# Kernel tuning notes

Hardware: AMD Instinct MI355X
Metric: run time of the kernel (lower is better)

The kernel has to match this reference:

```python
import jax, jax.numpy as jnp
import numpy as np


def _conv1(x, w, b):
    # 1x1x1 Conv3d on [B, C, T, H, W]: pure channel mixing.
    return jnp.einsum('bcthw,oc->bothw', x, w) + b[None, :, None, None, None]


def setup_inputs() -> dict:
    key = jax.random.key(0)
    B, T, C, H, W = 4, 7, 64, 64, 64
    C2 = C // 2  # nf // scale
    ks = jax.random.split(key, 16)
    inp = {"x": jax.random.normal(ks[0], (B, T, C, H, W), jnp.float32)}
    i = 1
    for p in ("hw", "c", "t"):
        for name in ("theta", "phi", "g"):
            inp[f"{p}_{name}_w"] = jax.random.normal(ks[i], (C2, C), jnp.float32) * 0.05
            inp[f"{p}_{name}_b"] = jnp.zeros((C2,), jnp.float32)
            i += 1
        inp[f"{p}_z_w"] = jax.random.normal(ks[i], (C, C2), jnp.float32) * 0.05
        inp[f"{p}_z_b"] = jnp.zeros((C,), jnp.float32)
        i += 1
    return inp


def reference(x, hw_theta_w, hw_theta_b, hw_phi_w, hw_phi_b, hw_g_w, hw_g_b,
              hw_z_w, hw_z_b, c_theta_w, c_theta_b, c_phi_w, c_phi_b,
              c_g_w, c_g_b, c_z_w, c_z_b, t_theta_w, t_theta_b,
              t_phi_w, t_phi_b, t_g_w, t_g_b, t_z_w, t_z_b):
    B, T, C, H, W = x.shape
    HW = H * W
    xc = jnp.transpose(x, (0, 2, 1, 3, 4))  # [B, C, T, H, W]

    # ---- spatial (HW) non-local: tokens are H*W positions, feature dim C2*T ----
    th = _conv1(xc, hw_theta_w, hw_theta_b).reshape(B, -1, HW)  # [B, C2*T, HW]
    ph = _conv1(xc, hw_phi_w, hw_phi_b).reshape(B, -1, HW)
    g = _conv1(xc, hw_g_w, hw_g_b).reshape(B, -1, HW)
    f = jax.nn.softmax(jnp.einsum('bkp,bkq->bpq', th, ph), axis=-1)  # [B, HW, HW]
    y = jnp.einsum('bpq,bkq->bkp', f, g).reshape(B, -1, T, H, W)
    hw_z = _conv1(y, hw_z_w, hw_z_b)

    # ---- channel (C) non-local: tokens are C2 channels, feature dim T*H*W ----
    th = _conv1(xc, c_theta_w, c_theta_b).reshape(B, -1, T * HW)  # [B, C2, THW]
    ph = _conv1(xc, c_phi_w, c_phi_b).reshape(B, -1, T * HW)
    g = _conv1(xc, c_g_w, c_g_b).reshape(B, -1, T * HW)
    f = jax.nn.softmax(jnp.einsum('bin,bjn->bij', th, ph), axis=-1)  # [B, C2, C2]
    y = jnp.einsum('bij,bjn->bin', f, g).reshape(B, -1, T, H, W)
    c_z = _conv1(y, c_z_w, c_z_b)

    # ---- temporal (T) non-local: tokens are T frames, feature dim C2*H*W ----
    th = jnp.transpose(_conv1(xc, t_theta_w, t_theta_b), (0, 2, 1, 3, 4)).reshape(B, T, -1)
    ph = jnp.transpose(_conv1(xc, t_phi_w, t_phi_b), (0, 2, 1, 3, 4)).reshape(B, T, -1)
    g = jnp.transpose(_conv1(xc, t_g_w, t_g_b), (0, 2, 1, 3, 4)).reshape(B, T, -1)
    f = jax.nn.softmax(jnp.einsum('btd,bsd->bts', th, ph), axis=-1)  # [B, T, T]
    y = jnp.einsum('bts,bsd->btd', f, g).reshape(B, T, -1, H, W)
    t_z = _conv1(jnp.transpose(y, (0, 2, 1, 3, 4)), t_z_w, t_z_b)

    z = hw_z + c_z + t_z + xc  # [B, C, T, H, W]
    return jnp.transpose(z, (0, 2, 1, 3, 4))  # [B, T, C, H, W]
```

## Files before the change

### kernel.cpp

```cpp
#include <hip/hip_runtime.h>
#include <hip/hip_bf16.h>

typedef unsigned short u16;
typedef __attribute__((ext_vector_type(8))) short s16x8;
typedef __attribute__((ext_vector_type(4))) float f32x4;

#define B_    4
#define T_    7
#define C_    64
#define C2_   32
#define HW_   4096
#define KF_   224
#define NTOT_ 28672

__device__ __forceinline__ float bf2f(u16 v){ return __uint_as_float(((unsigned)v)<<16); }
__device__ __forceinline__ u16 f2bf(float f){
  unsigned u = __float_as_uint(f);
  u = u + 0x7fffu + ((u>>16)&1u);
  return (u16)(u>>16);
}

static const size_t OFF_TH_HW=0;
static const size_t OFF_PH_HW=7340032;
static const size_t OFF_G_HW =14680064;
static const size_t OFF_Y_HW =22020096;
static const size_t OFF_TH_T =29360128;
static const size_t OFF_PH_T =44040192;
static const size_t OFF_GRAM =58720256;
static const size_t OFF_SROW =58785792;
static const size_t OFF_LT   =58786816;
static const size_t OFF_MC   =58787840;
static const size_t OFF_VC   =58853376;
static const size_t OFF_MT   =58854400;
static const size_t OFF_VT   =58870784;

__global__ __launch_bounds__(256) void k1_proj(
    const float* __restrict__ x,
    const float* w0,const float* bb0,const float* w1,const float* bb1,
    const float* w2,const float* bb2,const float* w3,const float* bb3,
    const float* w4,const float* bb4,
    u16* o0,u16* o1,u16* o2,float* o3,float* o4)
{
  __shared__ float wsm[5][C2_][C_];
  __shared__ float bsm[5][C2_];
  const float* wp[5]={w0,w1,w2,w3,w4};
  const float* bp[5]={bb0,bb1,bb2,bb3,bb4};
  int tid=threadIdx.x;
  for(int e=tid;e<5*C2_*C_;e+=256){ int pr=e>>11; int rc=e&2047; wsm[pr][rc>>6][rc&63]=wp[pr][rc]; }
  if(tid<5*C2_) bsm[tid>>5][tid&31]=bp[tid>>5][tid&31];
  __syncthreads();
  int bi=blockIdx.x;
  int b=bi/112, r=bi%112, t=r>>4;
  int p=((r&15)<<8)+tid;
  const float* xp = x + (((long)(b*T_+t))*C_)*HW_ + p;
  float xc[C_];
  #pragma unroll
  for(int c=0;c<C_;c++) xc[c]=xp[(long)c*HW_];
  long okm  = ((long)b*KF_ + t)*HW_ + p;
  long otok = ((long)(b*HW_) + p)*KF_ + t;

  for(int pr=0;pr<5;pr++){
    for(int c2=0;c2<C2_;c2++){
      float acc=bsm[pr][c2];
      const float4* wr=(const float4*)wsm[pr][c2];
      #pragma unroll
      for(int q=0;q<16;q++){ float4 w4=wr[q];
        acc+=w4.x*xc[q*4]+w4.y*xc[q*4+1]+w4.z*xc[q*4+2]+w4.w*xc[q*4+3]; }
      if(pr==0)      o0[otok + c2*T_]=f2bf(acc);
      else if(pr==1) o1[otok + c2*T_]=f2bf(acc);
      else if(pr==2) o2[okm + (long)(c2*T_)*HW_]=f2bf(acc);
      else if(pr==3) o3[okm + (long)(c2*T_)*HW_]=acc;
      else           o4[okm + (long)(c2*T_)*HW_]=acc;
    }
  }
}

__global__ __launch_bounds__(256,2) void k2_attn(
    const u16* __restrict__ th_tok,
    const u16* __restrict__ ph_tok,
    const u16* __restrict__ g_km,
    u16* __restrict__ y_g)
{
  __shared__ __align__(16) u16 ph_s[64][228];
  __shared__ __align__(16) u16 g_s[224][68];
  __shared__ float den_s[64];
  int tid=threadIdx.x;
  int id=blockIdx.x;
  int b=(id&7)>>1;
  int n=((id>>3)<<1)|(id&1);
  int p0=n<<6;
  int lane=tid&63, wv=tid>>6;
  int qw=wv<<4;
  int m=lane&15, gq=lane>>4;

  s16x8 thB[7];
  {
    const u16* thp = th_tok + ((long)(b*HW_ + p0 + qw + m))*KF_ + 4*gq;
    #pragma unroll
    for(int st=0; st<7; st++){
      union { s16x8 v; uint2 d[2]; } u;
      u.d[0]=*(const uint2*)(thp + st*32);
      u.d[1]=*(const uint2*)(thp + st*32 + 16);
      thB[st]=u.v;
    }
  }

  f32x4 Yacc[14];
  #pragma unroll
  for(int ft=0;ft<14;ft++) Yacc[ft]=(f32x4){0.f,0.f,0.f,0.f};
  float denp=0.f;

  const u16* phb = ph_tok + ((long)(b*HW_))*KF_;
  const u16* gb  = g_km  + ((long)(b*KF_))*HW_;

  int prow=tid>>2, pc0=(tid&3)*56;
  int gro=tid>>3,  gc0=(tid&7)*8;
  uint4 rph[7], rg[7];

  #pragma unroll
  for(int q=0;q<7;q++) rph[q]=*(const uint4*)(phb + (long)prow*KF_ + pc0 + q*8);
  #pragma unroll
  for(int it=0;it<7;it++) rg[it]=*(const uint4*)(gb + (long)(it*32+gro)*HW_ + gc0);

  for(int tile=0; tile<64; tile++){
    __syncthreads();
    { u16* dst=&ph_s[prow][pc0];
      #pragma unroll
      for(int q=0;q<7;q++){
        *(uint2*)(dst+q*8)  =make_uint2(rph[q].x,rph[q].y);
        *(uint2*)(dst+q*8+4)=make_uint2(rph[q].z,rph[q].w);
      } }
    { 
      #pragma unroll
      for(int it=0;it<7;it++){
        u16* dst=&g_s[it*32+gro][gc0];
        *(uint2*)(dst)  =make_uint2(rg[it].x,rg[it].y);
        *(uint2*)(dst+4)=make_uint2(rg[it].z,rg[it].w);
      } }
    if(tile<63){
      int j1=(tile+1)<<6;
      #pragma unroll
      for(int q=0;q<7;q++) rph[q]=*(const uint4*)(phb + (long)(j1+prow)*KF_ + pc0 + q*8);
      #pragma unroll
      for(int it=0;it<7;it++) rg[it]=*(const uint4*)(gb + (long)(it*32+gro)*HW_ + j1 + gc0);
    }
    __syncthreads();

    f32x4 Dt[4];
    #pragma unroll
    for(int kt=0;kt<4;kt++) Dt[kt]=(f32x4){0.f,0.f,0.f,0.f};
    #pragma unroll
    for(int st=0; st<7; st++){
      #pragma unroll
      for(int kt=0; kt<4; kt++){
        const u16* ap=&ph_s[kt*16+m][st*32+4*gq];
        union { s16x8 v; uint2 d[2]; } ua;
        ua.d[0]=*(const uint2*)ap;
        ua.d[1]=*(const uint2*)(ap+16);
        Dt[kt]=__builtin_amdgcn_mfma_f32_16x16x32_bf16(ua.v, thB[st], Dt[kt], 0,0,0);
      }
    }
    #pragma unroll
    for(int kt=0;kt<4;kt++){
      #pragma unroll
      for(int r=0;r<4;r++){ float pe=__expf(Dt[kt][r]); Dt[kt][r]=pe; denp+=pe; }
    }
    union { s16x8 v; u16 e[8]; } pa01, pa23;
    #pragma unroll
    for(int r=0;r<4;r++){
      pa01.e[r]=f2bf(Dt[0][r]); pa01.e[r+4]=f2bf(Dt[1][r]);
      pa23.e[r]=f2bf(Dt[2][r]); pa23.e[r+4]=f2bf(Dt[3][r]);
    }
    #pragma unroll
    for(int ft=0; ft<14; ft++){
      const u16* gp=&g_s[ft*16+m][4*gq];
      union { s16x8 v; uint2 d[2]; } b0,b1;
      b0.d[0]=*(const uint2*)gp;      b0.d[1]=*(const uint2*)(gp+16);
      b1.d[0]=*(const uint2*)(gp+32); b1.d[1]=*(const uint2*)(gp+48);
      Yacc[ft]=__builtin_amdgcn_mfma_f32_16x16x32_bf16(pa01.v, b0.v, Yacc[ft], 0,0,0);
      Yacc[ft]=__builtin_amdgcn_mfma_f32_16x16x32_bf16(pa23.v, b1.v, Yacc[ft], 0,0,0);
    }
  }

  denp += __shfl_xor(denp, 16, 64);
  denp += __shfl_xor(denp, 32, 64);
  if(gq==0) den_s[qw+m]=denp;
  __syncthreads();
  float inv[4];
  #pragma unroll
  for(int r=0;r<4;r++) inv[r]=1.f/den_s[qw+4*gq+r];
  u16* yb = y_g + ((long)(b*KF_))*HW_ + p0 + qw + 4*gq;
  #pragma unroll
  for(int ft=0; ft<14; ft++){
    long fo=(long)(ft*16+m)*HW_;
    #pragma unroll
    for(int r=0;r<4;r++) yb[fo+r]=f2bf(Yacc[ft][r]*inv[r]);
  }
}

__global__ __launch_bounds__(256) void k3_gram(const float* __restrict__ x,
                                               float* __restrict__ G, float* __restrict__ srow)
{
  __shared__ __align__(8) float xt[C_][68];
  int tid=threadIdx.x;
  int b=blockIdx.x>>6, ch=blockIdx.x&63;
  int ci0=(tid>>4)*4, cj0=(tid&15)*4;
  float acc[4][4];
  #pragma unroll
  for(int di=0;di<4;di++){acc[di][0]=0;acc[di][1]=0;acc[di][2]=0;acc[di][3]=0;}
  float sp=0.f;
  for(int st=0; st<7; st++){
    int n0=ch*448+st*64;
    int t=n0>>12, hw0=n0&4095;
    __syncthreads();
    for(int e=tid;e<C_*32;e+=256){ int c=e>>5, nn=e&31;
      *(float2*)&xt[c][nn*2]=*(const float2*)&x[(((long)(b*T_+t))*C_+c)*HW_+hw0+nn*2]; }
    __syncthreads();
    if(tid<C_){
      float s=0.f;
      for(int n=0;n<64;n++) s+=xt[tid][n];
      sp+=s;
    }
    for(int n=0;n<64;n++){
      float av[4],bv[4];
      #pragma unroll
      for(int d=0;d<4;d++){ av[d]=xt[ci0+d][n]; bv[d]=xt[cj0+d][n]; }
      #pragma unroll
      for(int di=0;di<4;di++)
        #pragma unroll
        for(int dj=0;dj<4;dj++)
          acc[di][dj]+=av[di]*bv[dj];
    }
  }
  float* Gb=G+b*4096;
  #pragma unroll
  for(int di=0;di<4;di++)
    #pragma unroll
    for(int dj=0;dj<4;dj++)
      atomicAdd(&Gb[(ci0+di)*64+cj0+dj], acc[di][dj]);
  if(tid<C_) atomicAdd(&srow[b*64+tid], sp);
}

__global__ __launch_bounds__(256) void k4_prep(
  const float* __restrict__ G, const float* __restrict__ srow,
  const float* cthw,const float* cthb,const float* cphw,const float* cphb,
  const float* cgw,const float* cgb,const float* czw,const float* czb,
  const float* tgw,const float* tgb,const float* tzw,const float* tzb,
  float* Mc, float* vc, float* Mt, float* vt)
{
  __shared__ float Gl[64][65];
  __shared__ float A1[32][65];
  __shared__ float fl[32][33];
  __shared__ float B1[32][65];
  __shared__ float sv[64], uu[32], vv[32], fb[32];
  int tid=threadIdx.x, b=blockIdx.x;
  for(int e=tid;e<4096;e+=256) Gl[e>>6][e&63]=G[b*4096+e];
  if(tid<64) sv[tid]=srow[b*64+tid];
  __syncthreads();
  if(tid<32){
    float a=0,bp=0;
    for(int c=0;c<64;c++){ a+=cthw[tid*64+c]*sv[c]; bp+=cphw[tid*64+c]*sv[c]; }
    uu[tid]=a; vv[tid]=bp;
  }
  __syncthreads();
  for(int e=tid;e<2048;e+=256){ int i=e>>6,cp=e&63;
    float a=0;
    for(int c=0;c<64;c++) a+=cthw[i*64+c]*Gl[c][cp];
    A1[i][cp]=a;
  }
  __syncthreads();
  for(int e=tid;e<1024;e+=256){ int i=e>>5,j=e&31;
    float a=0;
    for(int cp=0;cp<64;cp++) a+=A1[i][cp]*cphw[j*64+cp];
    a+=uu[i]*cphb[j]+cthb[i]*vv[j]+(float)NTOT_*cthb[i]*cphb[j];
    fl[i][j]=a;
  }
  __syncthreads();
  if(tid<32){
    float mx=-1e30f;
    for(int j=0;j<32;j++) mx=fmaxf(mx,fl[tid][j]);
    float s=0;
    for(int j=0;j<32;j++){ float e2=__expf(fl[tid][j]-mx); fl[tid][j]=e2; s+=e2; }
    float invs=1.f/s;
    for(int j=0;j<32;j++) fl[tid][j]*=invs;
    float a=0;
    for(int j=0;j<32;j++) a+=fl[tid][j]*cgb[j];
    fb[tid]=a;
  }
  __syncthreads();
  for(int e=tid;e<2048;e+=256){ int i=e>>6,cp=e&63;
    float a=0;
    for(int j=0;j<32;j++) a+=fl[i][j]*cgw[j*64+cp];
    B1[i][cp]=a;
  }
  __syncthreads();
  for(int e=tid;e<4096;e+=256){ int c=e>>6,cp=e&63;
    float a=0;
    for(int i=0;i<32;i++) a+=czw[c*32+i]*B1[i][cp];
    Mc[b*4096+e]=a;
  }
  if(tid<64){
    float a=0;
    for(int i=0;i<32;i++) a+=czw[tid*32+i]*fb[i];
    vc[b*64+tid]=a+czb[tid];
  }
  if(b==0){
    for(int e=tid;e<4096;e+=256){ int c=e>>6,cp=e&63;
      float a=0;
      for(int i=0;i<32;i++) a+=tzw[c*32+i]*tgw[i*64+cp];
      Mt[e]=a;
    }
    if(tid<64){
      float a=0;
      for(int i=0;i<32;i++) a+=tzw[tid*32+i]*tgb[i];
      vt[tid]=a+tzb[tid];
    }
  }
}

__global__ __launch_bounds__(256) void k5_tlogit(const float* __restrict__ th,
                                                 const float* __restrict__ ph,
                                                 float* __restrict__ Lt)
{
  __shared__ float wsum[4];
  int tid=threadIdx.x;
  int bi=blockIdx.x;
  int b=bi/49, r=bi%49, t=r/7, s=r%7;
  const float* A =th+((long)b*C2_*T_+t)*HW_;
  const float* Bp=ph+((long)b*C2_*T_+s)*HW_;
  float part=0.f;
  for(int c2=0;c2<C2_;c2++){
    const float4* a4=(const float4*)(A +(long)c2*T_*HW_);
    const float4* b4=(const float4*)(Bp+(long)c2*T_*HW_);
    #pragma unroll
    for(int rr=0;rr<4;rr++){
      int idx=rr*256+tid;
      float4 av=a4[idx], bv=b4[idx];
      part+=av.x*bv.x+av.y*bv.y+av.z*bv.z+av.w*bv.w;
    }
  }
  for(int off=32;off>0;off>>=1) part+=__shfl_down(part,off,64);
  if((tid&63)==0) wsum[tid>>6]=part;
  __syncthreads();
  if(tid==0) Lt[bi]=wsum[0]+wsum[1]+wsum[2]+wsum[3];
}

__global__ __launch_bounds__(256) void k6_final(
  const float* __restrict__ x, const u16* __restrict__ y_hw,
  const float* __restrict__ Lt, const float* __restrict__ Mc, const float* __restrict__ vc,
  const float* __restrict__ Mt, const float* __restrict__ vt,
  const float* hzw, const float* hzb, float* __restrict__ out)
{
  __shared__ float Mcl[64][64];
  __shared__ float Mtl[64][64];
  __shared__ float Wzl[64][32];
  __shared__ float cst[64];
  __shared__ float ftr[8];
  __shared__ float raw[8];
  int tid=threadIdx.x;
  int bi=blockIdx.x;
  int b=bi/112, r=bi%112, t=r>>4;
  int p=((r&15)<<8)+tid;
  for(int e=tid;e<4096;e+=256){ Mcl[e>>6][e&63]=Mc[b*4096+e]; Mtl[e>>6][e&63]=Mt[e]; }
  for(int e=tid;e<2048;e+=256) Wzl[e>>5][e&31]=hzw[e];
  if(tid<64) cst[tid]=vc[b*64+tid]+vt[tid]+hzb[tid];
  if(tid<7) raw[tid]=Lt[b*49+t*7+tid];
  __syncthreads();
  if(tid==0){
    float mx=-1e30f;
    for(int s=0;s<7;s++) mx=fmaxf(mx,raw[s]);
    float ssum=0.f; float e7[7];
    #pragma unroll
    for(int s=0;s<7;s++){ e7[s]=__expf(raw[s]-mx); ssum+=e7[s]; }
    #pragma unroll
    for(int s=0;s<7;s++) ftr[s]=e7[s]/ssum;
  }
  __syncthreads();
  float xcol[64], xbar[64];
  #pragma unroll
  for(int c=0;c<64;c++) xbar[c]=0.f;
  for(int s=0;s<7;s++){
    float fs=ftr[s];
    const float* xp=x+(((long)(b*T_+s))*C_)*HW_+p;
    if(s==t){
      #pragma unroll
      for(int c=0;c<64;c++){ float v0=xp[(long)c*HW_]; xcol[c]=v0; xbar[c]+=fs*v0; }
    } else {
      #pragma unroll
      for(int c=0;c<64;c++){ float v0=xp[(long)c*HW_]; xbar[c]+=fs*v0; }
    }
  }
  float yv[32];
  const u16* yp=y_hw+((long)b*KF_+t)*HW_+p;
  #pragma unroll
  for(int c2=0;c2<32;c2++) yv[c2]=bf2f(yp[(long)(c2*T_)*HW_]);
  float* op=out+(((long)(b*T_+t))*C_)*HW_+p;
  #pragma unroll
  for(int c=0;c<64;c++){
    float a=xcol[c]+cst[c];
    const float4* wr=(const float4*)Wzl[c];
    #pragma unroll
    for(int q=0;q<8;q++){ float4 w4=wr[q];
      a+=w4.x*yv[q*4]+w4.y*yv[q*4+1]+w4.z*yv[q*4+2]+w4.w*yv[q*4+3]; }
    const float4* mr=(const float4*)Mcl[c];
    const float4* tr=(const float4*)Mtl[c];
    #pragma unroll
    for(int q=0;q<16;q++){
      float4 m4=mr[q], t4=tr[q];
      a+=m4.x*xcol[q*4]+m4.y*xcol[q*4+1]+m4.z*xcol[q*4+2]+m4.w*xcol[q*4+3];
      a+=t4.x*xbar[q*4]+t4.y*xbar[q*4+1]+t4.z*xbar[q*4+2]+t4.w*xbar[q*4+3];
    }
    op[(long)c*HW_]=a;
  }
}

extern "C" void kernel_launch(void* const* d_in, const int* in_sizes, int n_in,
                              void* d_out, int out_size, void* d_ws, size_t ws_size,
                              hipStream_t stream)
{
  (void)in_sizes; (void)n_in; (void)out_size; (void)ws_size;
  const float* x      =(const float*)d_in[0];
  const float* hw_th_w=(const float*)d_in[1];  const float* hw_th_b=(const float*)d_in[2];
  const float* hw_ph_w=(const float*)d_in[3];  const float* hw_ph_b=(const float*)d_in[4];
  const float* hw_g_w =(const float*)d_in[5];  const float* hw_g_b =(const float*)d_in[6];
  const float* hw_z_w =(const float*)d_in[7];  const float* hw_z_b =(const float*)d_in[8];
  const float* c_th_w =(const float*)d_in[9];  const float* c_th_b =(const float*)d_in[10];
  const float* c_ph_w =(const float*)d_in[11]; const float* c_ph_b =(const float*)d_in[12];
  const float* c_g_w  =(const float*)d_in[13]; const float* c_g_b  =(const float*)d_in[14];
  const float* c_z_w  =(const float*)d_in[15]; const float* c_z_b  =(const float*)d_in[16];
  const float* t_th_w =(const float*)d_in[17]; const float* t_th_b =(const float*)d_in[18];
  const float* t_ph_w =(const float*)d_in[19]; const float* t_ph_b =(const float*)d_in[20];
  const float* t_g_w  =(const float*)d_in[21]; const float* t_g_b  =(const float*)d_in[22];
  const float* t_z_w  =(const float*)d_in[23]; const float* t_z_b  =(const float*)d_in[24];

  char* wsb=(char*)d_ws;
  u16*   th_hw=(u16*)  (wsb+OFF_TH_HW);
  u16*   ph_hw=(u16*)  (wsb+OFF_PH_HW);
  u16*   g_hw =(u16*)  (wsb+OFF_G_HW);
  u16*   y_hw =(u16*)  (wsb+OFF_Y_HW);
  float* th_t =(float*)(wsb+OFF_TH_T);
  float* ph_t =(float*)(wsb+OFF_PH_T);
  float* G    =(float*)(wsb+OFF_GRAM);
  float* srow =(float*)(wsb+OFF_SROW);
  float* Lt   =(float*)(wsb+OFF_LT);
  float* Mc   =(float*)(wsb+OFF_MC);
  float* vc   =(float*)(wsb+OFF_VC);
  float* Mt   =(float*)(wsb+OFF_MT);
  float* vt   =(float*)(wsb+OFF_VT);

  hipMemsetAsync(wsb+OFF_GRAM, 0, 65536+1024, stream);

  k1_proj <<<448,256,0,stream>>>(x, hw_th_w,hw_th_b, hw_ph_w,hw_ph_b, hw_g_w,hw_g_b,
                                 t_th_w,t_th_b, t_ph_w,t_ph_b,
                                 th_hw,ph_hw,g_hw,th_t,ph_t);
  k3_gram <<<256,256,0,stream>>>(x,G,srow);
  k4_prep <<<4,  256,0,stream>>>(G,srow, c_th_w,c_th_b,c_ph_w,c_ph_b,c_g_w,c_g_b,c_z_w,c_z_b,
                                 t_g_w,t_g_b,t_z_w,t_z_b, Mc,vc,Mt,vt);
  k5_tlogit<<<196,256,0,stream>>>(th_t,ph_t,Lt);
  k2_attn <<<256,256,0,stream>>>(th_hw,ph_hw,g_hw,y_hw);
  k6_final<<<448,256,0,stream>>>(x,y_hw,Lt,Mc,vc,Mt,vt,hw_z_w,hw_z_b,(float*)d_out);
}
```

Before: 665.9 us.

## Rewrite final combine kernel with bf16 MFMA and vectorize token-layout projection stores

After: 624.0 us. 6.3% less time.

```diff
diff --git a/kernel.cpp b/kernel.cpp
--- a/kernel.cpp
+++ b/kernel.cpp
@@ -57,20 +57,38 @@
   #pragma unroll
   for(int c=0;c<C_;c++) xc[c]=xp[(long)c*HW_];
   long okm  = ((long)b*KF_ + t)*HW_ + p;
-  long otok = ((long)(b*HW_) + p)*KF_ + t;
-
-  for(int pr=0;pr<5;pr++){
+  long otok = ((long)(b*HW_) + p)*KF_ + t*C2_;
+
+  union { u16 e[32]; uint4 q[4]; } tbuf, pbuf;
+  #pragma unroll
+  for(int c2=0;c2<32;c2++){
+    float a0=bsm[0][c2], a1=bsm[1][c2];
+    const float4* w0r=(const float4*)wsm[0][c2];
+    const float4* w1r=(const float4*)wsm[1][c2];
+    #pragma unroll
+    for(int q=0;q<16;q++){
+      float4 wa=w0r[q], wb=w1r[q];
+      a0+=wa.x*xc[q*4]+wa.y*xc[q*4+1]+wa.z*xc[q*4+2]+wa.w*xc[q*4+3];
+      a1+=wb.x*xc[q*4]+wb.y*xc[q*4+1]+wb.z*xc[q*4+2]+wb.w*xc[q*4+3];
+    }
+    tbuf.e[c2]=f2bf(a0); pbuf.e[c2]=f2bf(a1);
+  }
+  {
+    u16* t0=o0+otok; u16* p0p=o1+otok;
+    #pragma unroll
+    for(int q=0;q<4;q++){ *(uint4*)(t0+q*8)=tbuf.q[q]; *(uint4*)(p0p+q*8)=pbuf.q[q]; }
+  }
+  for(int pr=2;pr<5;pr++){
     for(int c2=0;c2<C2_;c2++){
       float acc=bsm[pr][c2];
       const float4* wr=(const float4*)wsm[pr][c2];
       #pragma unroll
       for(int q=0;q<16;q++){ float4 w4=wr[q];
         acc+=w4.x*xc[q*4]+w4.y*xc[q*4+1]+w4.z*xc[q*4+2]+w4.w*xc[q*4+3]; }
-      if(pr==0)      o0[otok + c2*T_]=f2bf(acc);
-      else if(pr==1) o1[otok + c2*T_]=f2bf(acc);
-      else if(pr==2) o2[okm + (long)(c2*T_)*HW_]=f2bf(acc);
-      else if(pr==3) o3[okm + (long)(c2*T_)*HW_]=acc;
-      else           o4[okm + (long)(c2*T_)*HW_]=acc;
+      long oa = okm + (long)(c2*T_)*HW_;
+      if(pr==2)      o2[oa]=f2bf(acc);
+      else if(pr==3) o3[oa]=acc;
+      else           o4[oa]=acc;
     }
   }
 }
@@ -130,7 +148,7 @@
         *(uint2*)(dst+q*8)  =make_uint2(rph[q].x,rph[q].y);
         *(uint2*)(dst+q*8+4)=make_uint2(rph[q].z,rph[q].w);
       } }
-    { 
+    {
       #pragma unroll
       for(int it=0;it<7;it++){
         u16* dst=&g_s[it*32+gro][gc0];
@@ -345,72 +363,95 @@
   if(tid==0) Lt[bi]=wsum[0]+wsum[1]+wsum[2]+wsum[3];
 }
 
-__global__ __launch_bounds__(256) void k6_final(
+__global__ __launch_bounds__(512) void k6_final(
   const float* __restrict__ x, const u16* __restrict__ y_hw,
-  const float* __restrict__ Lt, const float* __restrict__ Mc, const float* __restrict__ vc,
-  const float* __restrict__ Mt, const float* __restrict__ vt,
-  const float* hzw, const float* hzb, float* __restrict__ out)
-{
-  __shared__ float Mcl[64][64];
-  __shared__ float Mtl[64][64];
-  __shared__ float Wzl[64][32];
+  const float* __restrict__ Lt, const float* __restrict__ Mc,
+  const float* __restrict__ vc, const float* __restrict__ Mt,
+  const float* __restrict__ vt, const float* __restrict__ hzw,
+  const float* __restrict__ hzb, float* __restrict__ out)
+{
+  __shared__ u16 Msm[64][164];
+  __shared__ u16 Vsm[64][164];
   __shared__ float cst[64];
-  __shared__ float ftr[8];
-  __shared__ float raw[8];
+  __shared__ float fsm[7][8];
   int tid=threadIdx.x;
   int bi=blockIdx.x;
-  int b=bi/112, r=bi%112, t=r>>4;
-  int p=((r&15)<<8)+tid;
-  for(int e=tid;e<4096;e+=256){ Mcl[e>>6][e&63]=Mc[b*4096+e]; Mtl[e>>6][e&63]=Mt[e]; }
-  for(int e=tid;e<2048;e+=256) Wzl[e>>5][e&31]=hzw[e];
+  int b=bi>>6;
+  int hw0=(bi&63)<<6;
+  for(int e=tid;e<64*160;e+=512){
+    int c=e/160, k=e-c*160;
+    float v;
+    if(k<32)       v=hzw[c*32+k];
+    else if(k<96)  v=Mc[b*4096 + c*64 + (k-32)];
+    else           v=Mt[c*64 + (k-96)];
+    Msm[c][k]=f2bf(v);
+  }
   if(tid<64) cst[tid]=vc[b*64+tid]+vt[tid]+hzb[tid];
-  if(tid<7) raw[tid]=Lt[b*49+t*7+tid];
-  __syncthreads();
-  if(tid==0){
-    float mx=-1e30f;
-    for(int s=0;s<7;s++) mx=fmaxf(mx,raw[s]);
-    float ssum=0.f; float e7[7];
-    #pragma unroll
-    for(int s=0;s<7;s++){ e7[s]=__expf(raw[s]-mx); ssum+=e7[s]; }
-    #pragma unroll
-    for(int s=0;s<7;s++) ftr[s]=e7[s]/ssum;
-  }
-  __syncthreads();
-  float xcol[64], xbar[64];
-  #pragma unroll
-  for(int c=0;c<64;c++) xbar[c]=0.f;
-  for(int s=0;s<7;s++){
-    float fs=ftr[s];
-    const float* xp=x+(((long)(b*T_+s))*C_)*HW_+p;
-    if(s==t){
-      #pragma unroll
-      for(int c=0;c<64;c++){ float v0=xp[(long)c*HW_]; xcol[c]=v0; xbar[c]+=fs*v0; }
-    } else {
-      #pragma unroll
-      for(int c=0;c<64;c++){ float v0=xp[(long)c*HW_]; xbar[c]+=fs*v0; }
-    }
-  }
-  float yv[32];
-  const u16* yp=y_hw+((long)b*KF_+t)*HW_+p;
-  #pragma unroll
-  for(int c2=0;c2<32;c2++) yv[c2]=bf2f(yp[(long)(c2*T_)*HW_]);
-  float* op=out+(((long)(b*T_+t))*C_)*HW_+p;
-  #pragma unroll
-  for(int c=0;c<64;c++){
-    float a=xcol[c]+cst[c];
-    const float4* wr=(const float4*)Wzl[c];
-    #pragma unroll
-    for(int q=0;q<8;q++){ float4 w4=wr[q];
-      a+=w4.x*yv[q*4]+w4.y*yv[q*4+1]+w4.z*yv[q*4+2]+w4.w*yv[q*4+3]; }
-    const float4* mr=(const float4*)Mcl[c];
-    const float4* tr=(const float4*)Mtl[c];
-    #pragma unroll
-    for(int q=0;q<16;q++){
-      float4 m4=mr[q], t4=tr[q];
-      a+=m4.x*xcol[q*4]+m4.y*xcol[q*4+1]+m4.z*xcol[q*4+2]+m4.w*xcol[q*4+3];
-      a+=t4.x*xbar[q*4]+t4.y*xbar[q*4+1]+t4.z*xbar[q*4+2]+t4.w*xbar[q*4+3];
-    }
-    op[(long)c*HW_]=a;
+  if(tid<7){
+    float raw[7], mx=-1e30f;
+    #pragma unroll
+    for(int s=0;s<7;s++){ raw[s]=Lt[b*49+tid*7+s]; mx=fmaxf(mx,raw[s]); }
+    float ss=0.f;
+    #pragma unroll
+    for(int s=0;s<7;s++){ raw[s]=__expf(raw[s]-mx); ss+=raw[s]; }
+    float inv=1.f/ss;
+    #pragma unroll
+    for(int s=0;s<7;s++) fsm[tid][s]=raw[s]*inv;
+  }
+  int lane=tid&63, wv=tid>>6;
+  int m=lane&15, gq=lane>>4;
+  int pt=wv&3, oh=wv>>2;
+  int px0=pt*16;
+  int o0r=oh*32, o1r=oh*32+16;
+  const float* xb = x + ((long)(b*T_))*C_*HW_ + hw0;
+  const u16*  yb = y_hw + ((long)(b*KF_))*HW_ + hw0;
+  float* ob = out + ((long)(b*T_))*C_*HW_ + hw0;
+  __syncthreads();
+
+  for(int t=0;t<7;t++){
+    if(t) __syncthreads();
+    for(int e=tid;e<2048;e+=512){
+      int c2=e>>6, j=e&63;
+      Vsm[j][c2]=yb[(long)(c2*7+t)*HW_ + j];
+    }
+    float ft0=fsm[t][0],ft1=fsm[t][1],ft2=fsm[t][2],ft3=fsm[t][3],
+          ft4=fsm[t][4],ft5=fsm[t][5],ft6=fsm[t][6];
+    for(int e=tid;e<4096;e+=512){
+      int c=e>>6, j=e&63;
+      long base=(long)c*HW_ + j;
+      float x0=xb[base], x1=xb[base+(long)C_*HW_], x2=xb[base+(long)(2*C_)*HW_],
+            x3=xb[base+(long)(3*C_)*HW_], x4=xb[base+(long)(4*C_)*HW_],
+            x5=xb[base+(long)(5*C_)*HW_], x6=xb[base+(long)(6*C_)*HW_];
+      float xa=ft0*x0+ft1*x1+ft2*x2+ft3*x3+ft4*x4+ft5*x5+ft6*x6;
+      float xt;
+      switch(t){ case 0: xt=x0; break; case 1: xt=x1; break; case 2: xt=x2; break;
+                 case 3: xt=x3; break; case 4: xt=x4; break; case 5: xt=x5; break;
+                 default: xt=x6; }
+      Vsm[j][32+c]=f2bf(xt);
+      Vsm[j][96+c]=f2bf(xa);
+    }
+    __syncthreads();
+    f32x4 D0=(f32x4){0.f,0.f,0.f,0.f}, D1=(f32x4){0.f,0.f,0.f,0.f};
+    #pragma unroll
+    for(int st=0;st<5;st++){
+      union{ s16x8 v; uint2 d[2]; } a0,a1,bv;
+      const u16* bp=&Vsm[px0+m][st*32+4*gq];
+      bv.d[0]=*(const uint2*)bp;  bv.d[1]=*(const uint2*)(bp+16);
+      const u16* ap0=&Msm[o0r+m][st*32+4*gq];
+      a0.d[0]=*(const uint2*)ap0; a0.d[1]=*(const uint2*)(ap0+16);
+      const u16* ap1=&Msm[o1r+m][st*32+4*gq];
+      a1.d[0]=*(const uint2*)ap1; a1.d[1]=*(const uint2*)(ap1+16);
+      D0=__builtin_amdgcn_mfma_f32_16x16x32_bf16(a0.v,bv.v,D0,0,0,0);
+      D1=__builtin_amdgcn_mfma_f32_16x16x32_bf16(a1.v,bv.v,D1,0,0,0);
+    }
+    #pragma unroll
+    for(int r=0;r<4;r++){
+      int c0=o0r+4*gq+r, c1=o1r+4*gq+r;
+      long i0=(long)(t*C_+c0)*HW_ + px0+m;
+      long i1=(long)(t*C_+c1)*HW_ + px0+m;
+      ob[i0]=D0[r]+cst[c0]+xb[i0];
+      ob[i1]=D1[r]+cst[c1]+xb[i1];
+    }
   }
 }
 
@@ -458,5 +499,5 @@
                                  t_g_w,t_g_b,t_z_w,t_z_b, Mc,vc,Mt,vt);
   k5_tlogit<<<196,256,0,stream>>>(th_t,ph_t,Lt);
   k2_attn <<<256,256,0,stream>>>(th_hw,ph_hw,g_hw,y_hw);
-  k6_final<<<448,256,0,stream>>>(x,y_hw,Lt,Mc,vc,Mt,vt,hw_z_w,hw_z_b,(float*)d_out);
-}
+  k6_final<<<256,512,0,stream>>>(x,y_hw,Lt,Mc,vc,Mt,vt,hw_z_w,hw_z_b,(float*)d_out);
+}
```
